# Optimization experiments

Hardware: AMD Instinct MI355X
Metric: run time of the kernel (lower is better)

The kernel has to match this reference:

```python
import jax, jax.numpy as jnp
import numpy as np

MEM_DIM = 2000
FEA_DIM = 256
SHRINK_THRES = 0.0025
EPS = 1e-06


def setup_inputs() -> dict:
    key = jax.random.key(0)
    k1, k2 = jax.random.split(key)
    x = jax.random.normal(k1, (65536, FEA_DIM), dtype=jnp.float32)
    stdv = 1.0 / np.sqrt(FEA_DIM)
    weight = jax.random.uniform(k2, (MEM_DIM, FEA_DIM), dtype=jnp.float32,
                                minval=-stdv, maxval=stdv)
    temperature = jnp.asarray(0.5, dtype=jnp.float32)
    return {"input": x, "weight": weight, "temperature": temperature}


def hard_shrink_relu(a, lambd=SHRINK_THRES, epsilon=EPS):
    a = jnp.clip(a, -10.0, 10.0)
    denom = jnp.maximum(jnp.abs(a - lambd) + epsilon, epsilon)
    out = jax.nn.relu(a - lambd) * a / denom
    return jnp.where(jnp.isnan(out) | jnp.isinf(out), 0.0, out)


def reference(input, weight, temperature):
    mem_dim = weight.shape[0]
    inv_m = 1.0 / mem_dim
    x = jnp.clip(input, -10.0, 10.0)                      # [N, F]
    att = jnp.einsum('nf,mf->nm', x, weight)              # [N, M]
    att = jax.nn.softmax(att / temperature, axis=1)
    # shrink_thres > 0 branch
    att = hard_shrink_relu(att)
    weight_sum = jnp.sum(att, axis=1, keepdims=True)      # [N, 1]
    zero_mask = weight_sum < 1e-08
    att = att / (weight_sum + 1e-08)
    att = jnp.where(zero_mask, inv_m, att)                # rows with ~zero sum -> uniform
    att = jnp.where(jnp.isnan(att) | jnp.isinf(att), inv_m, att)
    output = jnp.einsum('nm,mf->nf', att, weight)         # [N, F]
    return output, att
```

## Files before the change

kernel.cpp:

```cpp
#include <hip/hip_runtime.h>
#include <hip/hip_bf16.h>
#include <cstdint>

#define N_ROWS 65536
#define FEA    256
#define MEM    2000
#define MEMP   2048
#define LAMBD  0.0025f
#define SEPS   1e-6f
#define NW     16

typedef __attribute__((ext_vector_type(8))) _Float16 f16x8;
typedef __attribute__((ext_vector_type(8))) short    bf16x8;
typedef __attribute__((ext_vector_type(4))) float    f32x4;

__device__ __forceinline__ short f2bf(float f) {
    union { float f; uint32_t u; } v; v.f = f;
    uint32_t r = v.u + 0x7fffu + ((v.u >> 16) & 1u);
    return (short)(r >> 16);
}

__global__ __launch_bounds__(256) void prep_kernel(const float* __restrict__ W,
                                                   const float* __restrict__ temp,
                                                   _Float16* __restrict__ Whl2,
                                                   short* __restrict__ Wt) {
    __shared__ float tile[8][260];
    const int t  = threadIdx.x;
    const int m0 = blockIdx.x * 8;
    const int row = t >> 5, col = (t & 31) * 8;
    const int m = m0 + row;
    const float scale = 1.4426950408889634f / temp[0];
    if (m < MEM) {
        f32x4 a = *(const f32x4*)(W + (size_t)m * FEA + col);
        f32x4 b = *(const f32x4*)(W + (size_t)m * FEA + col + 4);
        #pragma unroll
        for (int u = 0; u < 4; ++u) { tile[row][col+u] = a[u]; tile[row][col+4+u] = b[u]; }
    } else {
        #pragma unroll
        for (int u = 0; u < 8; ++u) tile[row][col+u] = 0.f;
    }
    __syncthreads();
    {
        const int c = col >> 5, q = (col >> 3) & 3;
        const int tt = m >> 4, lr = m & 15;
        _Float16 hi[8], lo[8];
        #pragma unroll
        for (int j = 0; j < 8; ++j) {
            float w = tile[row][col + j] * scale;
            _Float16 h = (_Float16)w;
            hi[j] = h;
            lo[j] = (_Float16)((w - (float)h) * 2048.0f);
        }
        _Float16* dst = Whl2 + (((size_t)(tt * 8 + c)) << 10) + (q * 16 + lr) * 16;
        *(f16x8*)dst       = *(f16x8*)&hi[0];
        *(f16x8*)(dst + 8) = *(f16x8*)&lo[0];
    }
    {
        short buf[8];
        #pragma unroll
        for (int j = 0; j < 8; ++j) buf[j] = f2bf(tile[j][t]);
        *(bf16x8*)(Wt + (size_t)t * MEMP + m0) = *(bf16x8*)&buf[0];
    }
}

__global__ __launch_bounds__(1024, 4) void score_kernel(const float* __restrict__ x,
                                                        const _Float16* __restrict__ Whl2,
                                                        float* __restrict__ att) {
    __shared__ __align__(16) _Float16 ah_s[32][264];
    __shared__ __align__(16) _Float16 al_s[32][264];
    __shared__ __align__(16) _Float16 a2_s[32][264];
    __shared__ float redbuf[NW][32];
    __shared__ float redglob[2][32];

    const int tid  = threadIdx.x;
    const int lane = tid & 63;
    const int wid  = tid >> 6;
    const int lr   = lane & 15;
    const int q    = lane >> 4;
    const size_t r0 = (size_t)blockIdx.x * 32;

    {
        const int srow = tid >> 5, scol = (tid & 31) * 8;
        const float* xp = x + (r0 + srow) * FEA + scol;
        f32x4 v0 = *(const f32x4*)xp;
        f32x4 v1 = *(const f32x4*)(xp + 4);
        _Float16 hbuf[8], lbuf[8], sbuf[8];
        #pragma unroll
        for (int w = 0; w < 4; ++w) {
            float f0 = fminf(fmaxf(v0[w], -10.f), 10.f);
            float f1 = fminf(fmaxf(v1[w], -10.f), 10.f);
            _Float16 h0 = (_Float16)f0, h1 = (_Float16)f1;
            hbuf[w]     = h0;
            hbuf[4 + w] = h1;
            lbuf[w]     = (_Float16)(f0 - (float)h0);
            lbuf[4 + w] = (_Float16)(f1 - (float)h1);
            sbuf[w]     = (_Float16)((float)h0 * (1.0f / 2048.0f));
            sbuf[4 + w] = (_Float16)((float)h1 * (1.0f / 2048.0f));
        }
        *(f16x8*)&ah_s[srow][scol] = *(f16x8*)&hbuf[0];
        *(f16x8*)&al_s[srow][scol] = *(f16x8*)&lbuf[0];
        *(f16x8*)&a2_s[srow][scol] = *(f16x8*)&sbuf[0];
    }
    __syncthreads();

    f32x4 acc[2][8];
    #pragma unroll
    for (int rg = 0; rg < 2; ++rg)
        #pragma unroll
        for (int jj = 0; jj < 8; ++jj) acc[rg][jj] = (f32x4){0.f, 0.f, 0.f, 0.f};

    #pragma unroll 1
    for (int c = 0; c < 8; ++c) {
        f16x8 ah[2], al[2], a2[2];
        #pragma unroll
        for (int rg = 0; rg < 2; ++rg) {
            ah[rg] = *(const f16x8*)&ah_s[rg * 16 + lr][c * 32 + q * 8];
            al[rg] = *(const f16x8*)&al_s[rg * 16 + lr][c * 32 + q * 8];
            a2[rg] = *(const f16x8*)&a2_s[rg * 16 + lr][c * 32 + q * 8];
        }
        #pragma unroll
        for (int jj = 0; jj < 8; ++jj) {
            const int t = wid + 16 * jj;
            const _Float16* bp = Whl2 + (((size_t)(t * 8 + c)) << 10) + lane * 16;
            f16x8 bh = *(const f16x8*)bp;
            f16x8 bl = *(const f16x8*)(bp + 8);
            #pragma unroll
            for (int rg = 0; rg < 2; ++rg) {
                acc[rg][jj] = __builtin_amdgcn_mfma_f32_16x16x32_f16(ah[rg], bh, acc[rg][jj], 0, 0, 0);
                acc[rg][jj] = __builtin_amdgcn_mfma_f32_16x16x32_f16(al[rg], bh, acc[rg][jj], 0, 0, 0);
                acc[rg][jj] = __builtin_amdgcn_mfma_f32_16x16x32_f16(a2[rg], bl, acc[rg][jj], 0, 0, 0);
            }
        }
    }

    const bool lastv = (wid < 13);

    auto xred = [&](float v[2][4], int bidx) {
        #pragma unroll
        for (int m = 1; m < 16; m <<= 1)
            #pragma unroll
            for (int rg = 0; rg < 2; ++rg)
                #pragma unroll
                for (int i = 0; i < 4; ++i)
                    v[rg][i] += __shfl_xor(v[rg][i], m, 64);
        if (lr == 0) {
            #pragma unroll
            for (int rg = 0; rg < 2; ++rg)
                #pragma unroll
                for (int i = 0; i < 4; ++i) redbuf[wid][rg * 16 + q * 4 + i] = v[rg][i];
        }
        __syncthreads();
        if (tid < 32) {
            float r = redbuf[0][tid];
            #pragma unroll
            for (int w = 1; w < NW; ++w) r += redbuf[w][tid];
            redglob[bidx][tid] = r;
        }
        __syncthreads();
        #pragma unroll
        for (int rg = 0; rg < 2; ++rg)
            #pragma unroll
            for (int i = 0; i < 4; ++i) v[rg][i] = redglob[bidx][rg * 16 + q * 4 + i];
    };

    #pragma unroll
    for (int jj = 0; jj < 8; ++jj) {
        const bool v = (jj < 7) || lastv;
        #pragma unroll
        for (int rg = 0; rg < 2; ++rg)
            #pragma unroll
            for (int i = 0; i < 4; ++i)
                acc[rg][jj][i] = v ? exp2f(acc[rg][jj][i]) : 0.0f;
    }

    float Z[2][4];
    #pragma unroll
    for (int rg = 0; rg < 2; ++rg)
        #pragma unroll
        for (int i = 0; i < 4; ++i) Z[rg][i] = 0.f;
    #pragma unroll
    for (int jj = 0; jj < 8; ++jj)
        #pragma unroll
        for (int rg = 0; rg < 2; ++rg)
            #pragma unroll
            for (int i = 0; i < 4; ++i) Z[rg][i] += acc[rg][jj][i];
    xred(Z, 0);

    #pragma unroll
    for (int rg = 0; rg < 2; ++rg)
        #pragma unroll
        for (int i = 0; i < 4; ++i) Z[rg][i] = __builtin_amdgcn_rcpf(Z[rg][i]);
    #pragma unroll
    for (int jj = 0; jj < 8; ++jj)
        #pragma unroll
        for (int rg = 0; rg < 2; ++rg)
            #pragma unroll
            for (int i = 0; i < 4; ++i) {
                float a = acc[rg][jj][i] * Z[rg][i];
                float d = a - LAMBD;
                float o = d * a * __builtin_amdgcn_rcpf(d + SEPS);
                acc[rg][jj][i] = (d > 0.f) ? o : 0.f;
            }

    float WS[2][4];
    #pragma unroll
    for (int rg = 0; rg < 2; ++rg)
        #pragma unroll
        for (int i = 0; i < 4; ++i) WS[rg][i] = 0.f;
    #pragma unroll
    for (int jj = 0; jj < 8; ++jj)
        #pragma unroll
        for (int rg = 0; rg < 2; ++rg)
            #pragma unroll
            for (int i = 0; i < 4; ++i) WS[rg][i] += acc[rg][jj][i];
    xred(WS, 1);

    const float inv_m = 1.0f / (float)MEM;
    float scl[2][4];
    bool  zr[2][4];
    #pragma unroll
    for (int rg = 0; rg < 2; ++rg)
        #pragma unroll
        for (int i = 0; i < 4; ++i) {
            scl[rg][i] = __builtin_amdgcn_rcpf(WS[rg][i] + 1e-8f);
            zr[rg][i]  = (WS[rg][i] < 1e-8f);
        }

    #pragma unroll
    for (int rg = 0; rg < 2; ++rg)
        #pragma unroll
        for (int i = 0; i < 4; ++i) {
            float* p = att + (r0 + rg * 16 + q * 4 + i) * (size_t)MEM + wid * 16 + lr;
            #pragma unroll
            for (int jj = 0; jj < 8; ++jj) {
                if (jj < 7 || lastv) {
                    float vv = zr[rg][i] ? inv_m : acc[rg][jj][i] * scl[rg][i];
                    p[jj * 256] = vv;
                }
            }
        }
}

__global__ __launch_bounds__(512) void gemm2_kernel(const float* __restrict__ att,
                                                    const short* __restrict__ Wt,
                                                    float* __restrict__ out) {
    __shared__ short Asm[2][128][40];
    __shared__ short Bsm[2][256][40];
    const int tid  = threadIdx.x;
    const int lane = tid & 63;
    const int wid  = tid >> 6;
    const int rg   = wid >> 2;
    const int cg   = wid & 3;
    const int lr   = lane & 15;
    const int lk   = (lane >> 4) * 8;
    const size_t r0 = (size_t)blockIdx.x * 128;

    const int sa_row = tid >> 2, sa_ko = (tid & 3) * 8;
    const int sb_f   = tid >> 1, sb_ko = (tid & 1) * 16;

    auto stage = [&](int buf, int kc) {
        const int k0 = kc * 32;
        {
            int k = k0 + sa_ko;
            short b[8];
            if (k < MEM) {
                const float* ap = att + (r0 + sa_row) * (size_t)MEM + k;
                f32x4 v0 = *(const f32x4*)ap;
                f32x4 v1 = *(const f32x4*)(ap + 4);
                #pragma unroll
                for (int u = 0; u < 4; ++u) { b[u] = f2bf(v0[u]); b[4+u] = f2bf(v1[u]); }
            } else {
                #pragma unroll
                for (int u = 0; u < 8; ++u) b[u] = 0;
            }
            *(bf16x8*)&Asm[buf][sa_row][sa_ko] = *(bf16x8*)&b[0];
        }
        {
            const short* wp = Wt + (size_t)sb_f * MEMP + k0 + sb_ko;
            bf16x8 b0 = *(const bf16x8*)wp;
            bf16x8 b1 = *(const bf16x8*)(wp + 8);
            *(bf16x8*)&Bsm[buf][sb_f][sb_ko]     = b0;
            *(bf16x8*)&Bsm[buf][sb_f][sb_ko + 8] = b1;
        }
    };

    f32x4 acc[4][4];
    #pragma unroll
    for (int i = 0; i < 4; ++i)
        #pragma unroll
        for (int j = 0; j < 4; ++j) acc[i][j] = (f32x4){0.f, 0.f, 0.f, 0.f};

    stage(0, 0);
    int cur = 0;
    for (int kc = 0; kc < 63; ++kc) {
        __syncthreads();
        if (kc + 1 < 63) stage(cur ^ 1, kc + 1);
        bf16x8 a_[4], b_[4];
        #pragma unroll
        for (int i = 0; i < 4; ++i) a_[i] = *(const bf16x8*)&Asm[cur][rg * 64 + i * 16 + lr][lk];
        #pragma unroll
        for (int j = 0; j < 4; ++j) b_[j] = *(const bf16x8*)&Bsm[cur][cg * 64 + j * 16 + lr][lk];
        #pragma unroll
        for (int i = 0; i < 4; ++i)
            #pragma unroll
            for (int j = 0; j < 4; ++j)
                acc[i][j] = __builtin_amdgcn_mfma_f32_16x16x32_bf16(a_[i], b_[j], acc[i][j], 0, 0, 0);
        cur ^= 1;
    }

    #pragma unroll
    for (int i = 0; i < 4; ++i)
        #pragma unroll
        for (int j = 0; j < 4; ++j)
            #pragma unroll
            for (int ii = 0; ii < 4; ++ii) {
                size_t row = r0 + rg * 64 + i * 16 + (lane >> 4) * 4 + ii;
                out[row * FEA + cg * 64 + j * 16 + lr] = acc[i][j][ii];
            }
}

extern "C" void kernel_launch(void* const* d_in, const int* in_sizes, int n_in,
                              void* d_out, int out_size, void* d_ws, size_t ws_size,
                              hipStream_t stream) {
    const float* x = (const float*)d_in[0];
    const float* W = (const float*)d_in[1];
    const float* T = (const float*)d_in[2];
    float* out = (float*)d_out;
    float* att = out + (size_t)N_ROWS * FEA;
    _Float16* Whl2 = (_Float16*)d_ws;
    short*    Wt   = (short*)((char*)d_ws + (2u << 20));

    prep_kernel<<<dim3(256), dim3(256), 0, stream>>>(W, T, Whl2, Wt);
    score_kernel<<<dim3(N_ROWS / 32), dim3(1024), 0, stream>>>(x, Whl2, att);
    gemm2_kernel<<<dim3(N_ROWS / 128), dim3(512), 0, stream>>>(att, Wt, out);
}
```

Baseline: 511.3 us.

## Stage attention as bf16 in workspace and expand to fp32 inside gemm2

The score kernel now writes the normalized attention matrix as bf16 into a workspace buffer instead of fp32 into the output. The second GEMM reads that bf16 buffer, feeds it to the MFMA tiles and also writes the fp32 expansion of each element into the att output. The aim is to replace the score kernel's scattered fp32 stores with coalesced vector stores from gemm2 and to halve the intermediate read. Total traffic stays roughly the same, the returned att values are rounded to bf16 precision, and the path only runs when the workspace holds about 260 MB.

```diff
diff --git a/kernel.cpp b/kernel.cpp
--- a/kernel.cpp
+++ b/kernel.cpp
@@ -18,6 +18,10 @@
     union { float f; uint32_t u; } v; v.f = f;
     uint32_t r = v.u + 0x7fffu + ((v.u >> 16) & 1u);
     return (short)(r >> 16);
+}
+__device__ __forceinline__ float bf2f(short s) {
+    union { uint32_t u; float f; } v; v.u = ((uint32_t)(uint16_t)s) << 16;
+    return v.f;
 }
 
 __global__ __launch_bounds__(256) void prep_kernel(const float* __restrict__ W,
@@ -63,9 +67,11 @@
     }
 }
 
-__global__ __launch_bounds__(1024, 4) void score_kernel(const float* __restrict__ x,
-                                                        const _Float16* __restrict__ Whl2,
-                                                        float* __restrict__ att) {
+template <bool STORE_BF16>
+__device__ __forceinline__ void score_body(const float* __restrict__ x,
+                                           const _Float16* __restrict__ Whl2,
+                                           float* __restrict__ att,
+                                           short* __restrict__ attb) {
     __shared__ __align__(16) _Float16 ah_s[32][264];
     __shared__ __align__(16) _Float16 al_s[32][264];
     __shared__ __align__(16) _Float16 a2_s[32][264];
@@ -230,15 +236,27 @@
     for (int rg = 0; rg < 2; ++rg)
         #pragma unroll
         for (int i = 0; i < 4; ++i) {
-            float* p = att + (r0 + rg * 16 + q * 4 + i) * (size_t)MEM + wid * 16 + lr;
+            const size_t rowoff = (r0 + rg * 16 + q * 4 + i) * (size_t)MEM + wid * 16 + lr;
             #pragma unroll
             for (int jj = 0; jj < 8; ++jj) {
                 if (jj < 7 || lastv) {
                     float vv = zr[rg][i] ? inv_m : acc[rg][jj][i] * scl[rg][i];
-                    p[jj * 256] = vv;
+                    if (STORE_BF16) attb[rowoff + jj * 256] = f2bf(vv);
+                    else            att [rowoff + jj * 256] = vv;
                 }
             }
         }
+}
+
+__global__ __launch_bounds__(1024, 4) void score_kernel(const float* __restrict__ x,
+                                                        const _Float16* __restrict__ Whl2,
+                                                        float* __restrict__ att) {
+    score_body<false>(x, Whl2, att, nullptr);
+}
+__global__ __launch_bounds__(1024, 4) void score_kernel_b(const float* __restrict__ x,
+                                                          const _Float16* __restrict__ Whl2,
+                                                          short* __restrict__ attb) {
+    score_body<true>(x, Whl2, nullptr, attb);
 }
 
 __global__ __launch_bounds__(512) void gemm2_kernel(const float* __restrict__ att,
@@ -319,6 +337,86 @@
             }
 }
 
+__global__ __launch_bounds__(512) void gemm2_kernel_b(const short* __restrict__ attb,
+                                                      const short* __restrict__ Wt,
+                                                      float* __restrict__ att,
+                                                      float* __restrict__ out) {
+    __shared__ short Asm[2][128][40];
+    __shared__ short Bsm[2][256][40];
+    const int tid  = threadIdx.x;
+    const int lane = tid & 63;
+    const int wid  = tid >> 6;
+    const int rg   = wid >> 2;
+    const int cg   = wid & 3;
+    const int lr   = lane & 15;
+    const int lk   = (lane >> 4) * 8;
+    const size_t r0 = (size_t)blockIdx.x * 128;
+
+    const int sa_row = tid >> 2, sa_ko = (tid & 3) * 8;
+    const int sb_f   = tid >> 1, sb_ko = (tid & 1) * 16;
+
+    auto stage = [&](int buf, int kc) {
+        const int k0 = kc * 32;
+        {
+            int k = k0 + sa_ko;
+            const size_t rowoff = (r0 + sa_row) * (size_t)MEM;
+            if (k < MEM) {
+                bf16x8 v = *(const bf16x8*)(attb + rowoff + k);
+                *(bf16x8*)&Asm[buf][sa_row][sa_ko] = v;
+                f32x4 e0, e1;
+                #pragma unroll
+                for (int u = 0; u < 4; ++u) { e0[u] = bf2f(v[u]); e1[u] = bf2f(v[4 + u]); }
+                *(f32x4*)(att + rowoff + k)     = e0;
+                *(f32x4*)(att + rowoff + k + 4) = e1;
+            } else {
+                bf16x8 z = {0,0,0,0,0,0,0,0};
+                *(bf16x8*)&Asm[buf][sa_row][sa_ko] = z;
+            }
+        }
+        {
+            const short* wp = Wt + (size_t)sb_f * MEMP + k0 + sb_ko;
+            bf16x8 b0 = *(const bf16x8*)wp;
+            bf16x8 b1 = *(const bf16x8*)(wp + 8);
+            *(bf16x8*)&Bsm[buf][sb_f][sb_ko]     = b0;
+            *(bf16x8*)&Bsm[buf][sb_f][sb_ko + 8] = b1;
+        }
+    };
+
+    f32x4 acc[4][4];
+    #pragma unroll
+    for (int i = 0; i < 4; ++i)
+        #pragma unroll
+        for (int j = 0; j < 4; ++j) acc[i][j] = (f32x4){0.f, 0.f, 0.f, 0.f};
+
+    stage(0, 0);
+    int cur = 0;
+    for (int kc = 0; kc < 63; ++kc) {
+        __syncthreads();
+        if (kc + 1 < 63) stage(cur ^ 1, kc + 1);
+        bf16x8 a_[4], b_[4];
+        #pragma unroll
+        for (int i = 0; i < 4; ++i) a_[i] = *(const bf16x8*)&Asm[cur][rg * 64 + i * 16 + lr][lk];
+        #pragma unroll
+        for (int j = 0; j < 4; ++j) b_[j] = *(const bf16x8*)&Bsm[cur][cg * 64 + j * 16 + lr][lk];
+        #pragma unroll
+        for (int i = 0; i < 4; ++i)
+            #pragma unroll
+            for (int j = 0; j < 4; ++j)
+                acc[i][j] = __builtin_amdgcn_mfma_f32_16x16x32_bf16(a_[i], b_[j], acc[i][j], 0, 0, 0);
+        cur ^= 1;
+    }
+
+    #pragma unroll
+    for (int i = 0; i < 4; ++i)
+        #pragma unroll
+        for (int j = 0; j < 4; ++j)
+            #pragma unroll
+            for (int ii = 0; ii < 4; ++ii) {
+                size_t row = r0 + rg * 64 + i * 16 + (lane >> 4) * 4 + ii;
+                out[row * FEA + cg * 64 + j * 16 + lr] = acc[i][j][ii];
+            }
+}
+
 extern "C" void kernel_launch(void* const* d_in, const int* in_sizes, int n_in,
                               void* d_out, int out_size, void* d_ws, size_t ws_size,
                               hipStream_t stream) {
@@ -329,8 +427,15 @@
     float* att = out + (size_t)N_ROWS * FEA;
     _Float16* Whl2 = (_Float16*)d_ws;
     short*    Wt   = (short*)((char*)d_ws + (2u << 20));
+    short*    attb = (short*)((char*)d_ws + (4u << 20));
+    const size_t need = (4ull << 20) + 2ull * N_ROWS * MEM;
 
     prep_kernel<<<dim3(256), dim3(256), 0, stream>>>(W, T, Whl2, Wt);
-    score_kernel<<<dim3(N_ROWS / 32), dim3(1024), 0, stream>>>(x, Whl2, att);
-    gemm2_kernel<<<dim3(N_ROWS / 128), dim3(512), 0, stream>>>(att, Wt, out);
-}
+    if (ws_size >= need) {
+        score_kernel_b<<<dim3(N_ROWS / 32), dim3(1024), 0, stream>>>(x, Whl2, attb);
+        gemm2_kernel_b<<<dim3(N_ROWS / 128), dim3(512), 0, stream>>>(attb, Wt, att, out);
+    } else {
+        score_kernel<<<dim3(N_ROWS / 32), dim3(1024), 0, stream>>>(x, Whl2, att);
+        gemm2_kernel<<<dim3(N_ROWS / 128), dim3(512), 0, stream>>>(att, Wt, out);
+    }
+}
```

Result: slower. 633.1 us (+23.8%).
